# Kernel optimization log

Measured on AMD Instinct MI355X. Metric: run time of the kernel, lower is better.

The kernel has to match this reference:

```python
import jax, jax.numpy as jnp
import numpy as np

B, S, H, NH = 2, 2048, 512, 8
DK = H // NH


def setup_inputs() -> dict:
    key = jax.random.key(0)
    ks = jax.random.split(key, 12)
    inp = {
        "query": jax.random.normal(ks[0], (B, S, H), dtype=jnp.float32),
        "key": jax.random.normal(ks[1], (B, S, H), dtype=jnp.float32),
        "value": jax.random.normal(ks[2], (B, S, H), dtype=jnp.float32),
        "bias": jax.random.normal(ks[3], (B, 1, S, S), dtype=jnp.float32),
        "mask": jax.random.randint(ks[4], (B, S), 0, 2, dtype=jnp.int32),
        "Wq": jax.random.normal(ks[5], (H, H), dtype=jnp.float32) * 0.02,
        "bq": jax.random.normal(ks[6], (H,), dtype=jnp.float32) * 0.02,
        "Wk": jax.random.normal(ks[7], (H, H), dtype=jnp.float32) * 0.02,
        "bk": jax.random.normal(ks[8], (H,), dtype=jnp.float32) * 0.02,
        "Wv": jax.random.normal(ks[9], (H, H), dtype=jnp.float32) * 0.02,
        "bv": jax.random.normal(ks[10], (H,), dtype=jnp.float32) * 0.02,
    }
    return inp


def reference(query, key, value, bias, mask, Wq, bq, Wk, bk, Wv, bv):
    b = query.shape[0]
    # torch nn.Linear: x @ W.T + b, then split heads -> [B, h, S, d_k]
    def proj(x, W, bb):
        y = x @ W.T + bb
        return y.reshape(b, -1, NH, DK).transpose(0, 2, 1, 3)

    q = proj(query, Wq, bq)
    k = proj(key, Wk, bk)
    v = proj(value, Wv, bv)

    score = jnp.einsum("bhqd,bhkd->bhqk", q, k) / np.sqrt(DK).astype(np.float32)
    # NOTE: the source swaps bias/mask when calling attention():
    #   the 0/1 mask is ADDED to the scores...
    mask_add = mask.reshape(b, 1, 1, -1).astype(score.dtype)
    score = score + mask_add
    #   ...and the float bias is used for the masked_fill (bias == 0 -> -1e30).
    score = jnp.where(bias == 0, jnp.asarray(-1e30, score.dtype), score)
    attn = jax.nn.softmax(score, axis=-1)  # dropout=None in the source call
    x = jnp.einsum("bhqk,bhkd->bhqd", attn, v)
    return x.transpose(0, 2, 1, 3).reshape(b, -1, NH * DK)
```

## Files before the change

### kernel.cpp

```cpp
#include <hip/hip_runtime.h>
#include <hip/hip_bf16.h>
#include <stdint.h>

#define B_  2
#define S_  2048
#define H_  512
#define NH_ 8
#define DK_ 64

typedef __bf16 bf16x8 __attribute__((ext_vector_type(8)));
typedef short  s16x4  __attribute__((ext_vector_type(4)));
typedef float  f32x4  __attribute__((ext_vector_type(4)));

static __device__ __forceinline__ uint32_t pk2(float a, float b) {
  __hip_bfloat162 h = __float22bfloat162_rn(float2{a, b});
  uint32_t u;
  __builtin_memcpy(&u, &h, 4);
  return u;
}

static __device__ __forceinline__ f32x4 mfma_k16(s16x4 a, s16x4 b, f32x4 c) {
#if defined(__HIP_DEVICE_COMPILE__)
  return __builtin_amdgcn_mfma_f32_16x16x16bf16_1k(a, b, c, 0, 0, 0);
#else
  (void)a; (void)b;
  return c;
#endif
}

typedef const __attribute__((address_space(1))) uint32_t* gas_t;
typedef __attribute__((address_space(3))) uint32_t* las_t;
static __device__ __forceinline__ void cp16(const void* g, void* l) {
  __builtin_amdgcn_global_load_lds((gas_t)g, (las_t)l, 16, 0, 0);
}

struct ProjArgs {
  const float* X[3];
  const float* W[3];
  const float* Bv[3];
  uint16_t*    O[3];
  const float* bias;
  const int*   mask;
  uint32_t*    zrow;
  float*       fmL;
};

__global__ __launch_bounds__(256) void prep_proj_kernel(ProjArgs pa) {
  __shared__ __align__(16) char psm[32768];
  int bid = blockIdx.x, t = threadIdx.x;

  if (bid >= 384) {
    if (bid < 896) {
      int rr = bid - 384;
      const float* base = pa.bias + (size_t)rr * 8 * 2048 + t * 8;
      uint4 a[8], b2[8];
#pragma unroll
      for (int i = 0; i < 8; i++) {
        const uint4* src = (const uint4*)(base + (size_t)i * 2048);
        a[i] = src[0]; b2[i] = src[1];
      }
      uint32_t (*wbuf)[4] = (uint32_t (*)[4])psm;
      int wv = t >> 6, ln = t & 63;
#pragma unroll
      for (int i = 0; i < 8; i++) {
        bool z = ((a[i].x << 1) == 0u) | ((a[i].y << 1) == 0u) |
                 ((a[i].z << 1) == 0u) | ((a[i].w << 1) == 0u) |
                 ((b2[i].x << 1) == 0u) | ((b2[i].y << 1) == 0u) |
                 ((b2[i].z << 1) == 0u) | ((b2[i].w << 1) == 0u);
        uint64_t m = __ballot(z);
        if (ln == 0) {
          uint32_t bits = 0;
#pragma unroll
          for (int c = 0; c < 8; c++)
            bits |= (uint32_t)(((m >> (8 * c)) & 0xFFull) != 0ull) << c;
          wbuf[i][wv] = bits;
        }
      }
      __syncthreads();
      if (t < 8)
        pa.zrow[rr * 8 + t] = wbuf[t][0] | (wbuf[t][1] << 8) |
                              (wbuf[t][2] << 16) | (wbuf[t][3] << 24);
    } else {
      const float LOG2E = 1.44269504088896340736f;
#pragma unroll
      for (int i = 0; i < 16; i++) {
        int idx = i * 256 + t;
        pa.fmL[idx] = (float)pa.mask[idx] * LOG2E;
      }
    }
    return;
  }

  int xcd = bid & 7, j = bid >> 3;
  int gi = ((j >> 2) << 3) | xcd;
  int dtile = j & 3;
  int mat = gi >> 5, mtile = gi & 31;
  int m0 = mtile * 128, n0 = dtile * 128;
  const float* X  = pa.X[mat];
  const float* Wt = pa.W[mat];
  const float* Bv = pa.Bv[mat];
  uint16_t*    O  = pa.O[mat];

  uint16_t (*Xs)[64] = (uint16_t (*)[64])psm;
  uint16_t (*Ws)[64] = (uint16_t (*)[64])(psm + 16384);

  int w = t >> 6, l = t & 63, lo = l & 15, g = l >> 4;
  int lr = l >> 4;
  int lc = l & 15;

  const float* Xp = X + (size_t)(m0 + w * 32 + lr) * 512 + lc * 4;
  const float* Wp = Wt + (size_t)(n0 + w * 32 + lr) * 512 + lc * 4;

  f32x4 acc[2][8];
#pragma unroll
  for (int st = 0; st < 2; st++)
#pragma unroll
    for (int dt = 0; dt < 8; dt++) acc[st][dt] = (f32x4){0.f, 0.f, 0.f, 0.f};

  float4 xa[8], wa2[8];
#pragma unroll
  for (int i = 0; i < 8; i++) xa[i] = *(const float4*)(Xp + (size_t)i * 4 * 512);
#pragma unroll
  for (int i = 0; i < 8; i++) wa2[i] = *(const float4*)(Wp + (size_t)i * 4 * 512);

  for (int kb = 0; kb < 8; kb++) {
#pragma unroll
    for (int i = 0; i < 8; i++) {
      int r = w * 32 + i * 4 + lr;
      int s0 = (lc >> 1) ^ (r & 7);
      uint2 pk{pk2(xa[i].x, xa[i].y), pk2(xa[i].z, xa[i].w)};
      *(uint2*)&Xs[r][s0 * 8 + (lc & 1) * 4] = pk;
    }
#pragma unroll
    for (int i = 0; i < 8; i++) {
      int r = w * 32 + i * 4 + lr;
      int s0 = (lc >> 1) ^ (r & 7);
      uint2 pk{pk2(wa2[i].x, wa2[i].y), pk2(wa2[i].z, wa2[i].w)};
      *(uint2*)&Ws[r][s0 * 8 + (lc & 1) * 4] = pk;
    }
    __syncthreads();
    if (kb < 7) {
      const float* Xn = Xp + (kb + 1) * 64;
      const float* Wn = Wp + (kb + 1) * 64;
#pragma unroll
      for (int i = 0; i < 8; i++) xa[i] = *(const float4*)(Xn + (size_t)i * 4 * 512);
#pragma unroll
      for (int i = 0; i < 8; i++) wa2[i] = *(const float4*)(Wn + (size_t)i * 4 * 512);
    }
#pragma unroll
    for (int kk = 0; kk < 2; kk++) {
      int seg = (kk * 4 + g) ^ (lo & 7);
      bf16x8 xf[2], wf[8];
#pragma unroll
      for (int st = 0; st < 2; st++)
        xf[st] = *(const bf16x8*)&Xs[w * 32 + st * 16 + lo][seg * 8];
#pragma unroll
      for (int dt = 0; dt < 8; dt++)
        wf[dt] = *(const bf16x8*)&Ws[dt * 16 + lo][seg * 8];
      if (mat < 2) {
#pragma unroll
        for (int st = 0; st < 2; st++)
#pragma unroll
          for (int dt = 0; dt < 8; dt++)
            acc[st][dt] = __builtin_amdgcn_mfma_f32_16x16x32_bf16(wf[dt], xf[st], acc[st][dt], 0, 0, 0);
      } else {
#pragma unroll
        for (int st = 0; st < 2; st++)
#pragma unroll
          for (int dt = 0; dt < 8; dt++)
            acc[st][dt] = __builtin_amdgcn_mfma_f32_16x16x32_bf16(xf[st], wf[dt], acc[st][dt], 0, 0, 0);
      }
    }
    __syncthreads();
  }

  if (mat < 2) {
    float scale = (mat == 0) ? 0.125f : 1.0f;
    float4 bv4[8];
#pragma unroll
    for (int dt = 0; dt < 8; dt++)
      bv4[dt] = *(const float4*)(Bv + n0 + dt * 16 + g * 4);
#pragma unroll
    for (int st = 0; st < 2; st++) {
      int ss = m0 + w * 32 + st * 16 + lo;
      int bb = ss >> 11, sIn = ss & 2047;
#pragma unroll
      for (int dt = 0; dt < 8; dt++) {
        int h2 = dtile * 2 + (dt >> 2);
        uint16_t* op = O + ((size_t)(bb * NH_ + h2) * S_ + sIn) * DK_ +
                       (dt & 3) * 16 + g * 4;
        float v0 = (acc[st][dt][0] + bv4[dt].x) * scale;
        float v1 = (acc[st][dt][1] + bv4[dt].y) * scale;
        float v2 = (acc[st][dt][2] + bv4[dt].z) * scale;
        float v3 = (acc[st][dt][3] + bv4[dt].w) * scale;
        uint2 pk{pk2(v0, v1), pk2(v2, v3)};
        *(uint2*)op = pk;
      }
    }
  } else {
    float bval[8];
#pragma unroll
    for (int dt = 0; dt < 8; dt++) bval[dt] = Bv[n0 + dt * 16 + lo];
#pragma unroll
    for (int st = 0; st < 2; st++) {
      int m = m0 + w * 32 + st * 16 + g * 4;
      int bb = m >> 11, sIn = m & 2047;
#pragma unroll
      for (int dt = 0; dt < 8; dt++) {
        int h2 = dtile * 2 + (dt >> 2);
        int dd = (dt & 3) * 16 + lo;
        float v0 = acc[st][dt][0] + bval[dt];
        float v1 = acc[st][dt][1] + bval[dt];
        float v2 = acc[st][dt][2] + bval[dt];
        float v3 = acc[st][dt][3] + bval[dt];
        uint2 pk{pk2(v0, v1), pk2(v2, v3)};
        *(uint2*)(O + ((size_t)(bb * NH_ + h2) * DK_ + dd) * S_ + sIn) = pk;
      }
    }
  }
}

__global__ __launch_bounds__(256) void attn_kernel(
    const uint16_t* __restrict__ Qb, const uint16_t* __restrict__ Kb,
    const uint16_t* __restrict__ Vt, const uint32_t* __restrict__ zrow,
    const float* __restrict__ fmL, const float* __restrict__ bias,
    float* __restrict__ out) {
  int bid = blockIdx.x;
  int bh = bid & 15, qtile = bid >> 4;
  int b = bh >> 3, h = bh & 7;
  int q0 = qtile * 64;
  int t = threadIdx.x;
  int w = t >> 6, l = t & 63, lo = l & 15, g = l >> 4;

  __shared__ __align__(16) char smem[57344];

  const uint16_t* Qh = Qb + (size_t)bh * S_ * DK_;
  const uint16_t* Kh = Kb + (size_t)bh * S_ * DK_;
  const uint16_t* Vh = Vt + (size_t)bh * DK_ * S_;

  int lrow = l >> 3, lseg = (l & 7) ^ lrow;
  const uint16_t* kbase = Kh + (size_t)(w * 16 + lrow) * DK_ + lseg * 8;
  const uint16_t* vbase = Vh + (size_t)(w * 16 + lrow) * S_ + lseg * 8;
  int kdo = w * 2048;
  int vdo = 8192 + w * 2048;

  float* fmlds = (float*)(smem + 49152);
  const float* fmG = fmL + b * S_;
  cp16(fmG + w * 256 + l * 4, smem + 49152 + w * 1024);
  cp16(fmG + 1024 + w * 256 + l * 4, smem + 49152 + 4096 + w * 1024);

  auto stage = [&](const uint16_t* kp, const uint16_t* vp, uint32_t bufo) {
    cp16(kp, smem + bufo + kdo);
    cp16(kp + 512, smem + bufo + kdo + 1024);
    cp16(vp, smem + bufo + vdo);
    cp16(vp + 8 * S_, smem + bufo + vdo + 1024);
  };
  stage(kbase, vbase, 0);
  stage(kbase + 4096, vbase + 64, 16384);
  const uint16_t* kpS = kbase + 8192;
  const uint16_t* vpS = vbase + 128;

  uint32_t zall = zrow[(b << 11) + q0 + l];
#pragma unroll
  for (int s = 1; s < 64; s <<= 1) zall |= __shfl_xor(zall, s);

  bf16x8 qf[4][2];
#pragma unroll
  for (int qt = 0; qt < 4; qt++)
#pragma unroll
    for (int kk = 0; kk < 2; kk++)
      qf[qt][kk] = *(const bf16x8*)(Qh + (size_t)(q0 + qt * 16 + lo) * DK_ + kk * 32 + g * 8);

  f32x4 o[4][4];
#pragma unroll
  for (int dt = 0; dt < 4; dt++)
#pragma unroll
    for (int qt = 0; qt < 4; qt++) o[dt][qt] = (f32x4){0.f, 0.f, 0.f, 0.f};
  f32x4 tsa[4];
#pragma unroll
  for (int qt = 0; qt < 4; qt++) tsa[qt] = (f32x4){0.f, 0.f, 0.f, 0.f};
  const s16x4 vone = {(short)0x3F80, (short)0x3F80, (short)0x3F80, (short)0x3F80};

  const float LOG2E = 1.44269504088896340736f;

  uint32_t oA = 0, oB = 16384, oC = 32768;

  for (int kb = 0; kb < 32; kb++) {
    int k0 = kb * 64;
    if (kb < 31) asm volatile("s_waitcnt vmcnt(4)" ::: "memory");
    else         asm volatile("s_waitcnt vmcnt(0)" ::: "memory");
    __builtin_amdgcn_s_barrier();
    if (kb + 2 < 32) {
      stage(kpS, vpS, oC);
      kpS += 4096; vpS += 64;
    }
    __builtin_amdgcn_sched_barrier(0);

    const uint16_t* KsT = (const uint16_t*)(smem + oA);
    const uint16_t* VsT = (const uint16_t*)(smem + oA + 8192);

    s16x4 vf[4];
    {
      int s = (2 * w + (g >> 1)) ^ (lo & 7);
      int off = s * 8 + (g & 1) * 4;
#pragma unroll
      for (int dt = 0; dt < 4; dt++)
        vf[dt] = *(const s16x4*)(VsT + (dt * 16 + lo) * 64 + off);
    }
    bf16x8 kf[2];
#pragma unroll
    for (int kk = 0; kk < 2; kk++) {
      int s = (kk * 4 + g) ^ (lo & 7);
      kf[kk] = *(const bf16x8*)(KsT + (w * 16 + lo) * 64 + s * 8);
    }

    f32x4 c[4];
#pragma unroll
    for (int qt = 0; qt < 4; qt++) {
      f32x4 z = {0.f, 0.f, 0.f, 0.f};
      z = __builtin_amdgcn_mfma_f32_16x16x32_bf16(kf[0], qf[qt][0], z, 0, 0, 0);
      c[qt] = __builtin_amdgcn_mfma_f32_16x16x32_bf16(kf[1], qf[qt][1], z, 0, 0, 0);
    }

    float4 mv4 = *(const float4*)(fmlds + kb * 64 + w * 16 + g * 4);
    s16x4 pf[4];
    if (((zall >> kb) & 1u) == 0u) {
#pragma unroll
      for (int qt = 0; qt < 4; qt++) {
        float p0 = __builtin_amdgcn_exp2f(__builtin_fmaf(c[qt][0], LOG2E, mv4.x));
        float p1 = __builtin_amdgcn_exp2f(__builtin_fmaf(c[qt][1], LOG2E, mv4.y));
        float p2 = __builtin_amdgcn_exp2f(__builtin_fmaf(c[qt][2], LOG2E, mv4.z));
        float p3 = __builtin_amdgcn_exp2f(__builtin_fmaf(c[qt][3], LOG2E, mv4.w));
        union { s16x4 v; uint32_t u[2]; } uu;
        uu.u[0] = pk2(p0, p1);
        uu.u[1] = pk2(p2, p3);
        pf[qt] = uu.v;
      }
    } else {
#pragma unroll
      for (int qt = 0; qt < 4; qt++) {
        float4 bz = *(const float4*)(bias + ((size_t)(b * S_ + q0 + qt * 16 + lo)) * S_ + k0 + w * 16 + g * 4);
        float p0 = (bz.x == 0.f) ? 0.f : __builtin_amdgcn_exp2f(__builtin_fmaf(c[qt][0], LOG2E, mv4.x));
        float p1 = (bz.y == 0.f) ? 0.f : __builtin_amdgcn_exp2f(__builtin_fmaf(c[qt][1], LOG2E, mv4.y));
        float p2 = (bz.z == 0.f) ? 0.f : __builtin_amdgcn_exp2f(__builtin_fmaf(c[qt][2], LOG2E, mv4.z));
        float p3 = (bz.w == 0.f) ? 0.f : __builtin_amdgcn_exp2f(__builtin_fmaf(c[qt][3], LOG2E, mv4.w));
        union { s16x4 v; uint32_t u[2]; } uu;
        uu.u[0] = pk2(p0, p1);
        uu.u[1] = pk2(p2, p3);
        pf[qt] = uu.v;
      }
    }

#pragma unroll
    for (int qt = 0; qt < 4; qt++)
      tsa[qt] = mfma_k16(vone, pf[qt], tsa[qt]);

#pragma unroll
    for (int dt = 0; dt < 4; dt++)
#pragma unroll
      for (int qt = 0; qt < 4; qt++)
        o[dt][qt] = mfma_k16(vf[dt], pf[qt], o[dt][qt]);

    uint32_t tmp = oA; oA = oB; oB = oC; oC = tmp;
  }

  float* OT = (float*)smem;
  float* LS = (float*)(smem + 8448);
  __syncthreads();
  if (g == 0) {
#pragma unroll
    for (int qt = 0; qt < 4; qt++) LS[(w * 4 + qt) * 16 + lo] = tsa[qt][0];
  }
#pragma unroll
  for (int qh = 0; qh < 2; qh++) {
#pragma unroll
    for (int ww = 0; ww < 4; ww++) {
      if (w == ww) {
#pragma unroll
        for (int dt = 0; dt < 4; dt++)
#pragma unroll
          for (int qt = 0; qt < 2; qt++)
#pragma unroll
            for (int r = 0; r < 4; r++) {
              int idx = (dt * 16 + g * 4 + r) * 33 + qt * 16 + lo;
              float val = o[dt][qh * 2 + qt][r];
              if (ww == 0) OT[idx] = val;
              else         OT[idx] += val;
            }
      }
      __syncthreads();
    }
    {
      int q = t >> 3, dseg = (t & 7) * 8;
      int qt2 = qh * 2 + (q >> 4), lo2 = q & 15;
      float lsum = LS[(0 * 4 + qt2) * 16 + lo2] + LS[(1 * 4 + qt2) * 16 + lo2] +
                   LS[(2 * 4 + qt2) * 16 + lo2] + LS[(3 * 4 + qt2) * 16 + lo2];
      float linv = 1.0f / fmaxf(lsum, 1e-30f);
      float* ob = out + ((size_t)(b * S_ + q0 + qh * 32 + q)) * H_ + h * DK_ + dseg;
#pragma unroll
      for (int i = 0; i < 2; i++) {
        float4 v;
        v.x = OT[(dseg + i * 4 + 0) * 33 + q] * linv;
        v.y = OT[(dseg + i * 4 + 1) * 33 + q] * linv;
        v.z = OT[(dseg + i * 4 + 2) * 33 + q] * linv;
        v.w = OT[(dseg + i * 4 + 3) * 33 + q] * linv;
        *(float4*)(ob + i * 4) = v;
      }
    }
    __syncthreads();
  }
}

extern "C" void kernel_launch(void* const* d_in, const int* in_sizes, int n_in,
                              void* d_out, int out_size, void* d_ws, size_t ws_size,
                              hipStream_t stream) {
  const float* query = (const float*)d_in[0];
  const float* key   = (const float*)d_in[1];
  const float* value = (const float*)d_in[2];
  const float* bias  = (const float*)d_in[3];
  const int*   mask  = (const int*)d_in[4];
  const float* Wq = (const float*)d_in[5];
  const float* bq = (const float*)d_in[6];
  const float* Wk = (const float*)d_in[7];
  const float* bk = (const float*)d_in[8];
  const float* Wv = (const float*)d_in[9];
  const float* bv = (const float*)d_in[10];

  char* ws = (char*)d_ws;
  uint32_t* zrow = (uint32_t*)ws;
  float*    fmL  = (float*)(ws + 16384);
  uint16_t* Qb = (uint16_t*)(ws + (size_t)(1 << 20));
  uint16_t* Kb = (uint16_t*)(ws + (size_t)(5 << 20));
  uint16_t* Vt = (uint16_t*)(ws + (size_t)(9 << 20));

  ProjArgs pa;
  pa.X[0] = query; pa.X[1] = key; pa.X[2] = value;
  pa.W[0] = Wq;    pa.W[1] = Wk;  pa.W[2] = Wv;
  pa.Bv[0] = bq;   pa.Bv[1] = bk; pa.Bv[2] = bv;
  pa.O[0] = Qb;    pa.O[1] = Kb;  pa.O[2] = Vt;
  pa.bias = bias;  pa.mask = mask;
  pa.zrow = zrow;  pa.fmL = fmL;

  prep_proj_kernel<<<897, 256, 0, stream>>>(pa);

  attn_kernel<<<512, 256, 0, stream>>>(Qb, Kb, Vt, zrow, fmL, bias, (float*)d_out);
}
```

Measured before the change: 157.8 us.

## Pre-convert projection inputs to bf16 and double-buffer GEMM via async LDS loads

Splits the fused prep+projection kernel in two. The first pass computes the bias zero-row bitmap and the mask scale, and also converts X and W from fp32 to bf16 in global memory. A separate projection GEMM kernel then streams the bf16 tiles straight into LDS with double-buffered global_load_lds copies, replacing the register-staged convert-and-store loop. This cuts conversion work and register pressure inside the GEMM and overlaps loads with MFMA. The cost is an extra kernel launch and an extra round trip through global memory for the bf16 copies (about 13 MB).

```diff
diff --git a/kernel.cpp b/kernel.cpp
--- a/kernel.cpp
+++ b/kernel.cpp
@@ -34,82 +34,111 @@
   __builtin_amdgcn_global_load_lds((gas_t)g, (las_t)l, 16, 0, 0);
 }
 
-struct ProjArgs {
+struct PrepArgs {
   const float* X[3];
   const float* W[3];
-  const float* Bv[3];
-  uint16_t*    O[3];
+  uint16_t*    Xb[3];
+  uint16_t*    Wb[3];
   const float* bias;
   const int*   mask;
   uint32_t*    zrow;
   float*       fmL;
 };
 
-__global__ __launch_bounds__(256) void prep_proj_kernel(ProjArgs pa) {
-  __shared__ __align__(16) char psm[32768];
+__global__ __launch_bounds__(256) void prep_a_kernel(PrepArgs pa) {
+  __shared__ uint32_t wbuf[8][4];
   int bid = blockIdx.x, t = threadIdx.x;
 
-  if (bid >= 384) {
-    if (bid < 896) {
-      int rr = bid - 384;
-      const float* base = pa.bias + (size_t)rr * 8 * 2048 + t * 8;
-      uint4 a[8], b2[8];
-#pragma unroll
-      for (int i = 0; i < 8; i++) {
-        const uint4* src = (const uint4*)(base + (size_t)i * 2048);
-        a[i] = src[0]; b2[i] = src[1];
-      }
-      uint32_t (*wbuf)[4] = (uint32_t (*)[4])psm;
-      int wv = t >> 6, ln = t & 63;
-#pragma unroll
-      for (int i = 0; i < 8; i++) {
-        bool z = ((a[i].x << 1) == 0u) | ((a[i].y << 1) == 0u) |
-                 ((a[i].z << 1) == 0u) | ((a[i].w << 1) == 0u) |
-                 ((b2[i].x << 1) == 0u) | ((b2[i].y << 1) == 0u) |
-                 ((b2[i].z << 1) == 0u) | ((b2[i].w << 1) == 0u);
-        uint64_t m = __ballot(z);
-        if (ln == 0) {
-          uint32_t bits = 0;
-#pragma unroll
-          for (int c = 0; c < 8; c++)
-            bits |= (uint32_t)(((m >> (8 * c)) & 0xFFull) != 0ull) << c;
-          wbuf[i][wv] = bits;
-        }
-      }
-      __syncthreads();
-      if (t < 8)
-        pa.zrow[rr * 8 + t] = wbuf[t][0] | (wbuf[t][1] << 8) |
-                              (wbuf[t][2] << 16) | (wbuf[t][3] << 24);
+  if (bid < 512) {
+    int rr = bid;
+    const float* base = pa.bias + (size_t)rr * 8 * 2048 + t * 8;
+    uint4 a[8], b2[8];
+#pragma unroll
+    for (int i = 0; i < 8; i++) {
+      const uint4* src = (const uint4*)(base + (size_t)i * 2048);
+      a[i] = src[0]; b2[i] = src[1];
+    }
+    int wv = t >> 6, ln = t & 63;
+#pragma unroll
+    for (int i = 0; i < 8; i++) {
+      bool z = ((a[i].x << 1) == 0u) | ((a[i].y << 1) == 0u) |
+               ((a[i].z << 1) == 0u) | ((a[i].w << 1) == 0u) |
+               ((b2[i].x << 1) == 0u) | ((b2[i].y << 1) == 0u) |
+               ((b2[i].z << 1) == 0u) | ((b2[i].w << 1) == 0u);
+      uint64_t m = __ballot(z);
+      if (ln == 0) {
+        uint32_t bits = 0;
+#pragma unroll
+        for (int c = 0; c < 8; c++)
+          bits |= (uint32_t)(((m >> (8 * c)) & 0xFFull) != 0ull) << c;
+        wbuf[i][wv] = bits;
+      }
+    }
+    __syncthreads();
+    if (t < 8)
+      pa.zrow[rr * 8 + t] = wbuf[t][0] | (wbuf[t][1] << 8) |
+                            (wbuf[t][2] << 16) | (wbuf[t][3] << 24);
+  } else if (bid < 944) {
+    int cid = bid - 512;
+    const float* src; uint16_t* dst; size_t off;
+    if (cid < 384) {
+      int mat = cid >> 7;
+      off = (size_t)(cid & 127) * 16384;
+      src = pa.X[mat]; dst = pa.Xb[mat];
     } else {
-      const float LOG2E = 1.44269504088896340736f;
-#pragma unroll
-      for (int i = 0; i < 16; i++) {
-        int idx = i * 256 + t;
-        pa.fmL[idx] = (float)pa.mask[idx] * LOG2E;
-      }
-    }
-    return;
-  }
-
+      int c2 = cid - 384;
+      int mat = c2 >> 4;
+      off = (size_t)(c2 & 15) * 16384;
+      src = pa.W[mat]; dst = pa.Wb[mat];
+    }
+    const float* s = src + off;
+    uint16_t*    d = dst + off;
+#pragma unroll
+    for (int i = 0; i < 8; i++) {
+      size_t e = (size_t)i * 2048 + t * 8;
+      float4 x0 = *(const float4*)(s + e);
+      float4 x1 = *(const float4*)(s + e + 4);
+      uint4 o4;
+      o4.x = pk2(x0.x, x0.y); o4.y = pk2(x0.z, x0.w);
+      o4.z = pk2(x1.x, x1.y); o4.w = pk2(x1.z, x1.w);
+      *(uint4*)(d + e) = o4;
+    }
+  } else {
+    const float LOG2E = 1.44269504088896340736f;
+#pragma unroll
+    for (int i = 0; i < 16; i++) {
+      int idx = i * 256 + t;
+      pa.fmL[idx] = (float)pa.mask[idx] * LOG2E;
+    }
+  }
+}
+
+struct GemmArgs {
+  const uint16_t* Xb[3];
+  const uint16_t* Wb[3];
+  const float*    Bv[3];
+  uint16_t*       O[3];
+};
+
+__global__ __launch_bounds__(256) void proj_kernel(GemmArgs ga) {
+  __shared__ __align__(16) char psm[65536];
+  int bid = blockIdx.x, t = threadIdx.x;
   int xcd = bid & 7, j = bid >> 3;
   int gi = ((j >> 2) << 3) | xcd;
   int dtile = j & 3;
   int mat = gi >> 5, mtile = gi & 31;
   int m0 = mtile * 128, n0 = dtile * 128;
-  const float* X  = pa.X[mat];
-  const float* Wt = pa.W[mat];
-  const float* Bv = pa.Bv[mat];
-  uint16_t*    O  = pa.O[mat];
-
-  uint16_t (*Xs)[64] = (uint16_t (*)[64])psm;
-  uint16_t (*Ws)[64] = (uint16_t (*)[64])(psm + 16384);
+  const uint16_t* X  = ga.Xb[mat];
+  const uint16_t* Wt = ga.Wb[mat];
+  const float*    Bv = ga.Bv[mat];
+  uint16_t*       O  = ga.O[mat];
 
   int w = t >> 6, l = t & 63, lo = l & 15, g = l >> 4;
-  int lr = l >> 4;
-  int lc = l & 15;
-
-  const float* Xp = X + (size_t)(m0 + w * 32 + lr) * 512 + lc * 4;
-  const float* Wp = Wt + (size_t)(n0 + w * 32 + lr) * 512 + lc * 4;
+
+  int lr8 = l >> 3;
+  int lsg = (l & 7) ^ lr8;
+  const uint16_t* xsrc = X  + (size_t)(m0 + w * 32 + lr8) * 512 + lsg * 8;
+  const uint16_t* wsrc = Wt + (size_t)(n0 + w * 32 + lr8) * 512 + lsg * 8;
 
   f32x4 acc[2][8];
 #pragma unroll
@@ -117,46 +146,38 @@
 #pragma unroll
     for (int dt = 0; dt < 8; dt++) acc[st][dt] = (f32x4){0.f, 0.f, 0.f, 0.f};
 
-  float4 xa[8], wa2[8];
-#pragma unroll
-  for (int i = 0; i < 8; i++) xa[i] = *(const float4*)(Xp + (size_t)i * 4 * 512);
-#pragma unroll
-  for (int i = 0; i < 8; i++) wa2[i] = *(const float4*)(Wp + (size_t)i * 4 * 512);
+  auto stage = [&](int kb, int buf) {
+    char* base = psm + buf * 32768;
+    int co = kb * 64;
+#pragma unroll
+    for (int i = 0; i < 4; i++) {
+      cp16(xsrc + (size_t)i * 8 * 512 + co, base + (w * 32 + i * 8) * 128);
+      cp16(wsrc + (size_t)i * 8 * 512 + co, base + 16384 + (w * 32 + i * 8) * 128);
+    }
+  };
+
+  stage(0, 0);
 
   for (int kb = 0; kb < 8; kb++) {
-#pragma unroll
-    for (int i = 0; i < 8; i++) {
-      int r = w * 32 + i * 4 + lr;
-      int s0 = (lc >> 1) ^ (r & 7);
-      uint2 pk{pk2(xa[i].x, xa[i].y), pk2(xa[i].z, xa[i].w)};
-      *(uint2*)&Xs[r][s0 * 8 + (lc & 1) * 4] = pk;
-    }
-#pragma unroll
-    for (int i = 0; i < 8; i++) {
-      int r = w * 32 + i * 4 + lr;
-      int s0 = (lc >> 1) ^ (r & 7);
-      uint2 pk{pk2(wa2[i].x, wa2[i].y), pk2(wa2[i].z, wa2[i].w)};
-      *(uint2*)&Ws[r][s0 * 8 + (lc & 1) * 4] = pk;
-    }
-    __syncthreads();
-    if (kb < 7) {
-      const float* Xn = Xp + (kb + 1) * 64;
-      const float* Wn = Wp + (kb + 1) * 64;
-#pragma unroll
-      for (int i = 0; i < 8; i++) xa[i] = *(const float4*)(Xn + (size_t)i * 4 * 512);
-#pragma unroll
-      for (int i = 0; i < 8; i++) wa2[i] = *(const float4*)(Wn + (size_t)i * 4 * 512);
-    }
+    int cur = kb & 1;
+    asm volatile("s_waitcnt vmcnt(0)" ::: "memory");
+    __builtin_amdgcn_s_barrier();
+    if (kb < 7) stage(kb + 1, cur ^ 1);
+    __builtin_amdgcn_sched_barrier(0);
+
+    const uint16_t* Xs = (const uint16_t*)(psm + cur * 32768);
+    const uint16_t* Ws = (const uint16_t*)(psm + cur * 32768 + 16384);
+
 #pragma unroll
     for (int kk = 0; kk < 2; kk++) {
       int seg = (kk * 4 + g) ^ (lo & 7);
       bf16x8 xf[2], wf[8];
 #pragma unroll
       for (int st = 0; st < 2; st++)
-        xf[st] = *(const bf16x8*)&Xs[w * 32 + st * 16 + lo][seg * 8];
+        xf[st] = *(const bf16x8*)(Xs + (w * 32 + st * 16 + lo) * 64 + seg * 8);
 #pragma unroll
       for (int dt = 0; dt < 8; dt++)
-        wf[dt] = *(const bf16x8*)&Ws[dt * 16 + lo][seg * 8];
+        wf[dt] = *(const bf16x8*)(Ws + (dt * 16 + lo) * 64 + seg * 8);
       if (mat < 2) {
 #pragma unroll
         for (int st = 0; st < 2; st++)
@@ -171,7 +192,6 @@
             acc[st][dt] = __builtin_amdgcn_mfma_f32_16x16x32_bf16(xf[st], wf[dt], acc[st][dt], 0, 0, 0);
       }
     }
-    __syncthreads();
   }
 
   if (mat < 2) {
@@ -432,16 +452,28 @@
   uint16_t* Qb = (uint16_t*)(ws + (size_t)(1 << 20));
   uint16_t* Kb = (uint16_t*)(ws + (size_t)(5 << 20));
   uint16_t* Vt = (uint16_t*)(ws + (size_t)(9 << 20));
-
-  ProjArgs pa;
+  uint16_t* Xb0 = (uint16_t*)(ws + (size_t)(16 << 20));
+  uint16_t* Xb1 = (uint16_t*)(ws + (size_t)(20 << 20));
+  uint16_t* Xb2 = (uint16_t*)(ws + (size_t)(24 << 20));
+  uint16_t* Wb0 = (uint16_t*)(ws + (size_t)(28 << 20));
+  uint16_t* Wb1 = (uint16_t*)(ws + (size_t)(29 << 20));
+  uint16_t* Wb2 = (uint16_t*)(ws + (size_t)(30 << 20));
+
+  PrepArgs pa;
   pa.X[0] = query; pa.X[1] = key; pa.X[2] = value;
   pa.W[0] = Wq;    pa.W[1] = Wk;  pa.W[2] = Wv;
-  pa.Bv[0] = bq;   pa.Bv[1] = bk; pa.Bv[2] = bv;
-  pa.O[0] = Qb;    pa.O[1] = Kb;  pa.O[2] = Vt;
+  pa.Xb[0] = Xb0;  pa.Xb[1] = Xb1; pa.Xb[2] = Xb2;
+  pa.Wb[0] = Wb0;  pa.Wb[1] = Wb1; pa.Wb[2] = Wb2;
   pa.bias = bias;  pa.mask = mask;
   pa.zrow = zrow;  pa.fmL = fmL;
 
-  prep_proj_kernel<<<897, 256, 0, stream>>>(pa);
-
+  GemmArgs ga;
+  ga.Xb[0] = Xb0; ga.Xb[1] = Xb1; ga.Xb[2] = Xb2;
+  ga.Wb[0] = Wb0; ga.Wb[1] = Wb1; ga.Wb[2] = Wb2;
+  ga.Bv[0] = bq;  ga.Bv[1] = bk;  ga.Bv[2] = bv;
+  ga.O[0] = Qb;   ga.O[1] = Kb;   ga.O[2] = Vt;
+
+  prep_a_kernel<<<945, 256, 0, stream>>>(pa);
+  proj_kernel<<<384, 256, 0, stream>>>(ga);
   attn_kernel<<<512, 256, 0, stream>>>(Qb, Kb, Vt, zrow, fmL, bias, (float*)d_out);
 }
```

Result: slower. 161.1 us (+2.1%).
